# Optimization experiments

Hardware: AMD Instinct MI355X
Metric: run time of the kernel (lower is better)

## Reference

```python
import jax, jax.numpy as jnp
import numpy as np

RES = 32  # voxel grid resolution per axis (cfg.MODEL.NEURAL_POINTS.VOXEL_RES)


def upsample_ac(x, s):
    """Bilinear upsample with align_corners=True. x: [B,C,h,w] -> [B,C,h*s,w*s]."""
    if s == 1:
        return x
    B, C, h, w = x.shape
    H, W = h * s, w * s
    ys = jnp.arange(H, dtype=x.dtype) * ((h - 1) / (H - 1))
    xs = jnp.arange(W, dtype=x.dtype) * ((w - 1) / (W - 1))
    y0 = jnp.floor(ys).astype(jnp.int32)
    x0 = jnp.floor(xs).astype(jnp.int32)
    y1 = jnp.minimum(y0 + 1, h - 1)
    x1 = jnp.minimum(x0 + 1, w - 1)
    wy = (ys - y0.astype(x.dtype))[:, None]  # [H,1]
    wx = (xs - x0.astype(x.dtype))[None, :]  # [1,W]
    top = x[:, :, y0, :]
    bot = x[:, :, y1, :]
    a = top[..., x0]; b = top[..., x1]; c = bot[..., x0]; d = bot[..., x1]
    return (a * (1 - wx) + b * wx) * (1 - wy) + (c * (1 - wx) + d * wx) * wy


def vox_closest(pos):
    """construct_vox_points_closest: per occupied voxel, index of point closest to
    the voxel's point centroid. pos: [N,3] -> [RES^3] int32 indices."""
    N = pos.shape[0]
    Vn = RES ** 3
    mn = pos.min(0)
    mx = pos.max(0)
    vsz = (mx - mn) / RES  # obtain_voxel_size_based_grid_res
    coord = jnp.clip(jnp.floor((pos - mn) / vsz).astype(jnp.int32), 0, RES - 1)
    vid = (coord[:, 0] * RES + coord[:, 1]) * RES + coord[:, 2]  # [N]
    cnt = jax.ops.segment_sum(jnp.ones((N,), pos.dtype), vid, Vn)
    cen = jax.ops.segment_sum(pos, vid, Vn) / jnp.maximum(cnt, 1.0)[:, None]
    d = jnp.sum((pos - cen[vid]) ** 2, axis=-1)  # [N] dist^2 to own-voxel centroid
    dmin = jax.ops.segment_min(d, vid, Vn)
    cand = jnp.where(d <= dmin[vid], jnp.arange(N, dtype=jnp.int32), N)
    midx = jax.ops.segment_min(cand, vid, Vn)
    return jnp.where(midx >= N, 0, midx)  # guard (rare) empty voxels


def reference(rgb, f1, f2, f3, points_pos, points_dir, W1, b1, W2, b2, points_mask):
    V, _, H, W = rgb.shape
    N = V * H * W
    C = 59
    # valid_index = where(points_mask == 1) (mask is all ones -> identity gather)
    valid = jnp.nonzero(points_mask[0] == 1, size=N, fill_value=0)[0]
    pos = points_pos[0, valid]          # [N,3]
    pdir = points_dir[0, valid]         # [N,3]
    # project_point_feats: upsample each pyramid level to full res, concat channels
    ups = [upsample_ac(rgb, 1), upsample_ac(f1, 2), upsample_ac(f2, 4), upsample_ac(f3, 8)]
    pif = jnp.concatenate(ups, axis=1)                       # [V,59,H,W]
    pif = jnp.transpose(pif, (0, 2, 3, 1)).reshape(N, C)     # [N,59]
    color = jax.lax.stop_gradient(jnp.transpose(rgb, (0, 2, 3, 1)).reshape(N, 3))
    pif = pif[valid]
    color = color[valid]
    emb = jnp.concatenate([pif, pdir], axis=-1)              # [N,62]
    midx = vox_closest(pos)                                  # [32768]
    sel_emb = emb[midx]
    sel_pos = pos[midx]
    sel_color = color[midx]
    sel_dir = pdir[midx]
    # point_mlp (premlp_init): 62 -> 256 -> 256
    h = jax.nn.relu(sel_emb @ W1 + b1)
    points_embedding = h @ W2 + b2
    return points_embedding, sel_pos, sel_color, sel_dir


def setup_inputs() -> dict:
    key = jax.random.key(0)
    ks = jax.random.split(key, 10)
    V, H, W = 8, 240, 320
    N = V * H * W
    return {
        "rgb": jax.random.uniform(ks[0], (V, 3, H, W), jnp.float32),
        "f1": jax.random.normal(ks[1], (V, 8, H // 2, W // 2), jnp.float32),
        "f2": jax.random.normal(ks[2], (V, 16, H // 4, W // 4), jnp.float32),
        "f3": jax.random.normal(ks[3], (V, 32, H // 8, W // 8), jnp.float32),
        "points_pos": jax.random.uniform(ks[4], (1, N, 3), jnp.float32),
        "points_dir": jax.random.normal(ks[5], (1, N, 3), jnp.float32),
        "W1": jax.random.normal(ks[6], (62, 256), jnp.float32) * 0.05,
        "b1": jnp.zeros((256,), jnp.float32),
        "W2": jax.random.normal(ks[7], (256, 256), jnp.float32) * 0.05,
        "b2": jnp.zeros((256,), jnp.float32),
        "points_mask": jnp.ones((1, N), jnp.int32),
    }
```

## Files before the change

kernel.cpp:

```cpp
#include <hip/hip_runtime.h>
#include <hip/hip_bf16.h>
#include <limits.h>
#include <stddef.h>

#define NPTS   614400
#define RESV   32
#define NVOX   (RESV*RESV*RESV)
#define IMG_H  240
#define IMG_W  320
#define IMG_HW (IMG_H*IMG_W)
#define INF    __builtin_inff()
#define CAP    64
#define SPILLCAP 4096

typedef __attribute__((ext_vector_type(8))) short short8;
typedef __attribute__((ext_vector_type(4))) short s16x4;
typedef __attribute__((ext_vector_type(4))) float f32x4;
typedef float f32x4u __attribute__((ext_vector_type(4), aligned(4)));

__device__ __forceinline__ float fadd_(float a, float b){
#pragma clang fp contract(off)
  return a + b;
}
__device__ __forceinline__ float fsub_(float a, float b){
#pragma clang fp contract(off)
  return a - b;
}
__device__ __forceinline__ float fmul_(float a, float b){
#pragma clang fp contract(off)
  return a * b;
}
__device__ __forceinline__ float fdiv_(float a, float b){
#pragma clang fp contract(off)
  return a / b;
}

__device__ __forceinline__ short f2bf(float x){
  __hip_bfloat16 h = __float2bfloat16(x);
  return *reinterpret_cast<short*>(&h);
}

__global__ void k_prep(int* __restrict__ cnt, int* __restrict__ spillcnt,
                       const float* __restrict__ W1, const float* __restrict__ W2,
                       short* __restrict__ W1t, short* __restrict__ W2t,
                       const float* __restrict__ pos,
                       f32x4* __restrict__ pmin, f32x4* __restrict__ pmax){
  int gid = blockIdx.x*blockDim.x + threadIdx.x;
  if (gid < NVOX) cnt[gid] = 0;
  if (gid == 0) *spillcnt = 0;
  if (gid < 256*64){
    int n = gid >> 6, k = gid & 63;
    W1t[gid] = (k < 62) ? f2bf(W1[k*256 + n]) : (short)0;
  } else if (gid < 256*64 + 256*256){
    int j = gid - 256*64;
    int n = j >> 8, k = j & 255;
    W2t[j] = f2bf(W2[k*256 + n]);
  }

  const f32x4* p4 = (const f32x4*)pos;
  float mn[3] = {  INF,  INF,  INF };
  float mx[3] = { -INF, -INF, -INF };
  int stride = gridDim.x*blockDim.x;
  for (int t = gid; t < NPTS/4; t += stride){
    f32x4 a = p4[3*t+0], b = p4[3*t+1], c = p4[3*t+2];
    mn[0] = fminf(mn[0], fminf(fminf(a.x, a.w), fminf(b.z, c.y)));
    mx[0] = fmaxf(mx[0], fmaxf(fmaxf(a.x, a.w), fmaxf(b.z, c.y)));
    mn[1] = fminf(mn[1], fminf(fminf(a.y, b.x), fminf(b.w, c.z)));
    mx[1] = fmaxf(mx[1], fmaxf(fmaxf(a.y, b.x), fmaxf(b.w, c.z)));
    mn[2] = fminf(mn[2], fminf(fminf(a.z, b.y), fminf(c.x, c.w)));
    mx[2] = fmaxf(mx[2], fmaxf(fmaxf(a.z, b.y), fmaxf(c.x, c.w)));
  }
  #pragma unroll
  for (int off = 32; off >= 1; off >>= 1){
    #pragma unroll
    for (int c = 0; c < 3; c++){
      mn[c] = fminf(mn[c], __shfl_down(mn[c], off, 64));
      mx[c] = fmaxf(mx[c], __shfl_down(mx[c], off, 64));
    }
  }
  __shared__ float smn[4][3], smx[4][3];
  int lane = threadIdx.x & 63, w = threadIdx.x >> 6;
  if (lane == 0){
    #pragma unroll
    for (int c = 0; c < 3; c++){ smn[w][c] = mn[c]; smx[w][c] = mx[c]; }
  }
  __syncthreads();
  if (threadIdx.x == 0){
    f32x4 a, b;
    a.x = fminf(fminf(smn[0][0], smn[1][0]), fminf(smn[2][0], smn[3][0]));
    a.y = fminf(fminf(smn[0][1], smn[1][1]), fminf(smn[2][1], smn[3][1]));
    a.z = fminf(fminf(smn[0][2], smn[1][2]), fminf(smn[2][2], smn[3][2]));
    a.w = 0.f;
    b.x = fmaxf(fmaxf(smx[0][0], smx[1][0]), fmaxf(smx[2][0], smx[3][0]));
    b.y = fmaxf(fmaxf(smx[0][1], smx[1][1]), fmaxf(smx[2][1], smx[3][1]));
    b.z = fmaxf(fmaxf(smx[0][2], smx[1][2]), fmaxf(smx[2][2], smx[3][2]));
    b.w = 0.f;
    pmin[blockIdx.x] = a;
    pmax[blockIdx.x] = b;
  }
}

__device__ __forceinline__ void reduce_minmax(const f32x4* __restrict__ pmin,
                                              const f32x4* __restrict__ pmax,
                                              float mn[3], float vsz[3]){
  int t = threadIdx.x;
  f32x4 a = pmin[t], b = pmin[t+256];
  f32x4 c = pmax[t], d = pmax[t+256];
  float lmn[3] = { fminf(a.x,b.x), fminf(a.y,b.y), fminf(a.z,b.z) };
  float lmx[3] = { fmaxf(c.x,d.x), fmaxf(c.y,d.y), fmaxf(c.z,d.z) };
  #pragma unroll
  for (int off = 32; off >= 1; off >>= 1){
    #pragma unroll
    for (int k = 0; k < 3; k++){
      lmn[k] = fminf(lmn[k], __shfl_xor(lmn[k], off, 64));
      lmx[k] = fmaxf(lmx[k], __shfl_xor(lmx[k], off, 64));
    }
  }
  __shared__ float smn[4][3], smx[4][3];
  int lane = t & 63, w = t >> 6;
  if (lane == 0){
    #pragma unroll
    for (int k = 0; k < 3; k++){ smn[w][k] = lmn[k]; smx[w][k] = lmx[k]; }
  }
  __syncthreads();
  #pragma unroll
  for (int k = 0; k < 3; k++){
    mn[k] = fminf(fminf(smn[0][k], smn[1][k]), fminf(smn[2][k], smn[3][k]));
    float mx = fmaxf(fmaxf(smx[0][k], smx[1][k]), fmaxf(smx[2][k], smx[3][k]));
    vsz[k] = fdiv_(fsub_(mx, mn[k]), 32.0f);
  }
}

__global__ void k_scatter(const float* __restrict__ pos,
                          const f32x4* __restrict__ pmin, const f32x4* __restrict__ pmax,
                          int* __restrict__ cnt, int* __restrict__ slots,
                          int* __restrict__ spillcnt, int2* __restrict__ spill){
  float mn[3], vsz[3];
  reduce_minmax(pmin, pmax, mn, vsz);

  int t = blockIdx.x*blockDim.x + threadIdx.x;
  const f32x4* p4 = (const f32x4*)pos;
  f32x4 a = p4[3*t+0], b = p4[3*t+1], c = p4[3*t+2];
  float X[4] = {a.x, a.w, b.z, c.y};
  float Y[4] = {a.y, b.x, b.w, c.z};
  float Z[4] = {a.z, b.y, c.x, c.w};
  #pragma unroll
  for (int j = 0; j < 4; j++){
    int i = 4*t + j;
    float P[3] = {X[j], Y[j], Z[j]};
    int v = 0;
    #pragma unroll
    for (int k = 0; k < 3; k++){
      float tt = fdiv_(fsub_(P[k], mn[k]), vsz[k]);
      int cc = (int)floorf(tt);
      cc = min(max(cc, 0), RESV-1);
      v = v*RESV + cc;
    }
    int p = atomicAdd(&cnt[v], 1);
    if (p < CAP){
      slots[v*CAP + p] = i;
    } else {
      int sp = atomicAdd(spillcnt, 1);
      if (sp < SPILLCAP){ int2 e; e.x = v; e.y = i; spill[sp] = e; }
    }
  }
}

__launch_bounds__(256)
__global__ void k_voxfull(const int* __restrict__ cnt, const int* __restrict__ slots,
                          const int* __restrict__ spillcnt, const int2* __restrict__ spill,
                          const float* __restrict__ pos,
                          const float* __restrict__ pdir, const float* __restrict__ rgb,
                          const float* __restrict__ f1, const float* __restrict__ f2,
                          const float* __restrict__ f3,
                          float* __restrict__ selpos, float* __restrict__ selcol,
                          float* __restrict__ seldir, short* __restrict__ emb){
  int lane = threadIdx.x & 63;
  int v = blockIdx.x*4 + (threadIdx.x >> 6);
  int n = cnt[v];
  int m = 0;
  unsigned long long ball = 0;
  float px = 0.f, py = 0.f, pz = 0.f;

  if (n > CAP){
    if (lane == 0){
      int sc = min(*spillcnt, SPILLCAP);
      float sx = 0.f, sy = 0.f, sz = 0.f; int last = -1;
      for (int i = 0; i < n; i++){
        int best = INT_MAX;
        for (int j = 0; j < CAP; j++){
          int id = slots[v*CAP + j];
          if (id > last && id < best) best = id;
        }
        for (int j = 0; j < sc; j++){
          int2 e = spill[j];
          if (e.x == v && e.y > last && e.y < best) best = e.y;
        }
        sx = fadd_(sx, pos[3*best+0]);
        sy = fadd_(sy, pos[3*best+1]);
        sz = fadd_(sz, pos[3*best+2]);
        last = best;
      }
      float cf = (float)n;
      float cx = fdiv_(sx, cf), cy = fdiv_(sy, cf), cz = fdiv_(sz, cf);
      float dmin = INF; int mm = 0;
      for (int j = 0; j < CAP + sc; j++){
        int id; int ok = 1;
        if (j < CAP) id = slots[v*CAP + j];
        else { int2 e = spill[j-CAP]; ok = (e.x == v); id = e.y; }
        if (!ok) continue;
        float dx = fsub_(pos[3*id+0], cx);
        float dy = fsub_(pos[3*id+1], cy);
        float dz = fsub_(pos[3*id+2], cz);
        float d  = fadd_(fadd_(fmul_(dx,dx), fmul_(dy,dy)), fmul_(dz,dz));
        if (d < dmin || (d == dmin && id < mm)){ dmin = d; mm = id; }
      }
      m = mm;
    }
    m = __shfl(m, 0, 64);
  } else {
    int key = INT_MAX;
    float gx = 0.f, gy = 0.f, gz = 0.f;
    if (lane < n){
      key = slots[v*CAP + lane];
      if (key < NPTS-1){
        f32x4u q = *(const f32x4u*)&pos[3*key];
        gx = q.x; gy = q.y; gz = q.z;
      } else {
        gx = pos[3*key+0]; gy = pos[3*key+1]; gz = pos[3*key+2];
      }
    }
    int src = lane;
    #pragma unroll
    for (int k = 2; k <= 64; k <<= 1){
      #pragma unroll
      for (int j = k >> 1; j >= 1; j >>= 1){
        int ok = __shfl_xor(key, j, 64);
        int os = __shfl_xor(src, j, 64);
        bool up    = ((lane & k) == 0);
        bool lower = ((lane & j) == 0);
        bool sw = (lower == up) ? (ok < key) : (ok > key);
        if (sw){ key = ok; src = os; }
      }
    }
    px = __shfl(gx, src, 64);
    py = __shfl(gy, src, 64);
    pz = __shfl(gz, src, 64);

    float sx = 0.f, sy = 0.f, sz = 0.f;
    for (int i = 0; i < n; i++){
      sx = fadd_(sx, __shfl(px, i, 64));
      sy = fadd_(sy, __shfl(py, i, 64));
      sz = fadd_(sz, __shfl(pz, i, 64));
    }
    float cf = fmaxf((float)n, 1.0f);
    float cx = fdiv_(sx, cf), cy = fdiv_(sy, cf), cz = fdiv_(sz, cf);

    float bd = INF; int bi = 0;
    if (lane < n){
      float dx = fsub_(px, cx), dy = fsub_(py, cy), dz = fsub_(pz, cz);
      bd = fadd_(fadd_(fmul_(dx,dx), fmul_(dy,dy)), fmul_(dz,dz));
      bi = key;
    }
    #pragma unroll
    for (int off = 32; off >= 1; off >>= 1){
      float od = __shfl_xor(bd, off, 64);
      int   oi = __shfl_xor(bi, off, 64);
      if (od < bd || (od == bd && oi < bi)){ bd = od; bi = oi; }
    }
    m = bi;
    ball = __ballot(lane < n && key == m);
  }

  float wx_ = 0.f, wy_ = 0.f, wz_ = 0.f;
  if (ball){
    int wl = (int)(__ffsll((long long)ball) - 1);
    wx_ = __shfl(px, wl, 64);
    wy_ = __shfl(py, wl, 64);
    wz_ = __shfl(pz, wl, 64);
  }

  int img = m / IMG_HW;
  int rem = m - img*IMG_HW;
  int y = rem / IMG_W;
  int x = rem - y*IMG_W;
  int ch = lane;
  float val;
  if (ch < 3){
    val = rgb[((img*3 + ch)*IMG_H + y)*IMG_W + x];
    selcol[3*v+ch] = val;
    float sp = ball ? ((ch == 0) ? wx_ : (ch == 1) ? wy_ : wz_) : pos[3*m+ch];
    selpos[3*v+ch] = sp;
  } else if (ch < 59){
    int lvl = (ch >= 27) ? 2 : ((ch >= 11) ? 1 : 0);
    const float* f = (lvl == 0) ? f1 : ((lvl == 1) ? f2 : f3);
    int c   = ch - ((lvl == 0) ? 3 : ((lvl == 1) ? 11 : 27));
    int C   = 8 << lvl;
    int h   = 120 >> lvl, w = 160 >> lvl;
    float ry = (lvl == 0) ? (119.0f/239.0f) : ((lvl == 1) ? (59.0f/239.0f) : (29.0f/239.0f));
    float rx = (lvl == 0) ? (159.0f/319.0f) : ((lvl == 1) ? (79.0f/319.0f) : (39.0f/319.0f));
    float ys = (float)y * ry;
    float xs = (float)x * rx;
    int y0 = (int)floorf(ys);
    int x0 = (int)floorf(xs);
    int y1 = min(y0+1, h-1);
    int x1 = min(x0+1, w-1);
    float wy = ys - (float)y0;
    float wx = xs - (float)x0;
    const float* plane = f + ((size_t)img*C + c)*(size_t)(h*w);
    float aa = plane[y0*w + x0];
    float bb = plane[y0*w + x1];
    float cc = plane[y1*w + x0];
    float dd = plane[y1*w + x1];
    val = (aa*(1.f-wx) + bb*wx)*(1.f-wy) + (cc*(1.f-wx) + dd*wx)*wy;
  } else if (ch < 62){
    val = pdir[3*m + (ch-59)];
    seldir[3*v+(ch-59)] = val;
  } else {
    val = 0.f;
  }
  emb[(size_t)v*64 + ch] = f2bf(val);
}

#define MLP_BLOCKS 512
#define MLP_TILES  (NVOX/16/MLP_BLOCKS)
__launch_bounds__(256, 2)
__global__ void k_mlp(const short* __restrict__ emb, const short* __restrict__ W1t,
                      const float* __restrict__ b1f, const short* __restrict__ W2t,
                      const float* __restrict__ b2f, float* __restrict__ out){
  __shared__ short Hs[16][264];
  int t    = threadIdx.x;
  int lane = t & 63;
  int wv   = t >> 6;
  int m    = lane & 15;
  int q    = lane >> 4;

  short8 w1f[4][2], w2f[4][8];
  float  b1r[4][4], b2r[4];
  #pragma unroll
  for (int nt = 0; nt < 4; nt++){
    int n = wv*64 + nt*16 + m;
    #pragma unroll
    for (int kq = 0; kq < 2; kq++)
      w1f[nt][kq] = *(const short8*)&W1t[(size_t)n*64 + kq*32 + q*8];
    #pragma unroll
    for (int kq = 0; kq < 8; kq++)
      w2f[nt][kq] = *(const short8*)&W2t[(size_t)n*256 + kq*32 + q*8];
    #pragma unroll
    for (int i = 0; i < 4; i++)
      b1r[nt][i] = b1f[wv*64 + nt*16 + q*4 + i];
    b2r[nt] = b2f[n];
  }

  for (int tt = 0; tt < MLP_TILES; tt++){
    int row0 = (blockIdx.x*MLP_TILES + tt)*16;

    short8 ef0 = *(const short8*)&emb[(size_t)(row0 + m)*64 + q*8];
    short8 ef1 = *(const short8*)&emb[(size_t)(row0 + m)*64 + 32 + q*8];

    #pragma unroll
    for (int nt = 0; nt < 4; nt++){
      f32x4 c = {0.f, 0.f, 0.f, 0.f};
      c = __builtin_amdgcn_mfma_f32_16x16x32_bf16(w1f[nt][0], ef0, c, 0, 0, 0);
      c = __builtin_amdgcn_mfma_f32_16x16x32_bf16(w1f[nt][1], ef1, c, 0, 0, 0);
      s16x4 hv;
      #pragma unroll
      for (int i = 0; i < 4; i++)
        hv[i] = f2bf(fmaxf(c[i] + b1r[nt][i], 0.f));
      *(s16x4*)&Hs[m][wv*64 + nt*16 + q*4] = hv;
    }
    __syncthreads();

    f32x4 acc[4] = {{0,0,0,0},{0,0,0,0},{0,0,0,0},{0,0,0,0}};
    #pragma unroll
    for (int kq = 0; kq < 8; kq++){
      short8 af = *(const short8*)&Hs[m][kq*32 + q*8];
      #pragma unroll
      for (int nt = 0; nt < 4; nt++)
        acc[nt] = __builtin_amdgcn_mfma_f32_16x16x32_bf16(af, w2f[nt][kq], acc[nt], 0, 0, 0);
    }
    __syncthreads();

    #pragma unroll
    for (int nt = 0; nt < 4; nt++){
      int n = wv*64 + nt*16 + m;
      #pragma unroll
      for (int i = 0; i < 4; i++)
        out[(size_t)(row0 + q*4 + i)*256 + n] = acc[nt][i] + b2r[nt];
    }
  }
}

extern "C" void kernel_launch(void* const* d_in, const int* in_sizes, int n_in,
                              void* d_out, int out_size, void* d_ws, size_t ws_size,
                              hipStream_t stream){
  const float* rgb  = (const float*)d_in[0];
  const float* f1   = (const float*)d_in[1];
  const float* f2   = (const float*)d_in[2];
  const float* f3   = (const float*)d_in[3];
  const float* pos  = (const float*)d_in[4];
  const float* pdir = (const float*)d_in[5];
  const float* W1   = (const float*)d_in[6];
  const float* b1   = (const float*)d_in[7];
  const float* W2   = (const float*)d_in[8];
  const float* b2   = (const float*)d_in[9];

  float* out      = (float*)d_out;
  float* out_emb  = out;
  float* out_pos  = out + (size_t)NVOX*256;
  float* out_col  = out_pos + (size_t)NVOX*3;
  float* out_dir  = out_col + (size_t)NVOX*3;

  char* w = (char*)d_ws;
  int*   spillcnt = (int*)w;       w += 64;
  f32x4* pmin     = (f32x4*)w;     w += (size_t)512*16;
  f32x4* pmax     = (f32x4*)w;     w += (size_t)512*16;
  int*   cnt      = (int*)w;       w += (size_t)NVOX*4;
  short* W1t      = (short*)w;     w += (size_t)256*64*2;
  short* W2t      = (short*)w;     w += (size_t)256*256*2;
  short* emb      = (short*)w;     w += (size_t)NVOX*64*2;
  int2*  spill    = (int2*)w;      w += (size_t)SPILLCAP*8;
  int*   slots    = (int*)w;       w += (size_t)NVOX*CAP*4;

  k_prep    <<<512,    256, 0, stream>>>(cnt, spillcnt, W1, W2, W1t, W2t, pos, pmin, pmax);
  k_scatter <<<NPTS/1024, 256, 0, stream>>>(pos, pmin, pmax, cnt, slots, spillcnt, spill);
  k_voxfull <<<NVOX/4, 256, 0, stream>>>(cnt, slots, spillcnt, spill,
                                         pos, pdir, rgb, f1, f2, f3,
                                         out_pos, out_col, out_dir, emb);
  k_mlp     <<<MLP_BLOCKS, 256, 0, stream>>>(emb, W1t, b1, W2t, b2, out_emb);
}
```

Baseline: 198.2 us.

## Split voxel kernel and bucket voxels by selected point index for gather locality

```diff
diff --git a/kernel.cpp b/kernel.cpp
--- a/kernel.cpp
+++ b/kernel.cpp
@@ -12,6 +12,9 @@
 #define INF    __builtin_inff()
 #define CAP    64
 #define SPILLCAP 4096
+#define NB     150
+#define CAPB   448
+#define OCAP   2048
 
 typedef __attribute__((ext_vector_type(8))) short short8;
 typedef __attribute__((ext_vector_type(4))) short s16x4;
@@ -40,14 +43,16 @@
   return *reinterpret_cast<short*>(&h);
 }
 
-__global__ void k_prep(int* __restrict__ cnt, int* __restrict__ spillcnt,
+__global__ void k_prep(int* __restrict__ cnt, int* __restrict__ ctrs,
+                       int* __restrict__ bcnt,
                        const float* __restrict__ W1, const float* __restrict__ W2,
                        short* __restrict__ W1t, short* __restrict__ W2t,
                        const float* __restrict__ pos,
                        f32x4* __restrict__ pmin, f32x4* __restrict__ pmax){
   int gid = blockIdx.x*blockDim.x + threadIdx.x;
   if (gid < NVOX) cnt[gid] = 0;
-  if (gid == 0) *spillcnt = 0;
+  if (gid < NB) bcnt[gid] = 0;
+  if (gid < 2) ctrs[gid] = 0;
   if (gid < 256*64){
     int n = gid >> 6, k = gid & 63;
     W1t[gid] = (k < 62) ? f2bf(W1[k*256 + n]) : (short)0;
@@ -134,7 +139,7 @@
 __global__ void k_scatter(const float* __restrict__ pos,
                           const f32x4* __restrict__ pmin, const f32x4* __restrict__ pmax,
                           int* __restrict__ cnt, int* __restrict__ slots,
-                          int* __restrict__ spillcnt, int2* __restrict__ spill){
+                          int* __restrict__ ctrs, int2* __restrict__ spill){
   float mn[3], vsz[3];
   reduce_minmax(pmin, pmax, mn, vsz);
 
@@ -160,21 +165,19 @@
     if (p < CAP){
       slots[v*CAP + p] = i;
     } else {
-      int sp = atomicAdd(spillcnt, 1);
+      int sp = atomicAdd(&ctrs[0], 1);
       if (sp < SPILLCAP){ int2 e; e.x = v; e.y = i; spill[sp] = e; }
     }
   }
 }
 
 __launch_bounds__(256)
-__global__ void k_voxfull(const int* __restrict__ cnt, const int* __restrict__ slots,
-                          const int* __restrict__ spillcnt, const int2* __restrict__ spill,
-                          const float* __restrict__ pos,
-                          const float* __restrict__ pdir, const float* __restrict__ rgb,
-                          const float* __restrict__ f1, const float* __restrict__ f2,
-                          const float* __restrict__ f3,
-                          float* __restrict__ selpos, float* __restrict__ selcol,
-                          float* __restrict__ seldir, short* __restrict__ emb){
+__global__ void k_voxA(const int* __restrict__ cnt, const int* __restrict__ slots,
+                       const int* __restrict__ ctrs, const int2* __restrict__ spill,
+                       const float* __restrict__ pos,
+                       float* __restrict__ selpos, int* __restrict__ midx,
+                       int* __restrict__ bcnt, int* __restrict__ blist,
+                       int* __restrict__ octr, int* __restrict__ olist){
   int lane = threadIdx.x & 63;
   int v = blockIdx.x*4 + (threadIdx.x >> 6);
   int n = cnt[v];
@@ -184,7 +187,7 @@
 
   if (n > CAP){
     if (lane == 0){
-      int sc = min(*spillcnt, SPILLCAP);
+      int sc = min(ctrs[0], SPILLCAP);
       float sx = 0.f, sy = 0.f, sz = 0.f; int last = -1;
       for (int i = 0; i < n; i++){
         int best = INT_MAX;
@@ -279,6 +282,46 @@
     wy_ = __shfl(py, wl, 64);
     wz_ = __shfl(pz, wl, 64);
   }
+  if (lane < 3){
+    float sp = ball ? ((lane == 0) ? wx_ : (lane == 1) ? wy_ : wz_) : pos[3*m+lane];
+    selpos[3*v+lane] = sp;
+  }
+  if (lane == 0){
+    midx[v] = m;
+    int b = m >> 12;
+    int s = atomicAdd(&bcnt[b], 1);
+    if (s < CAPB) blist[b*CAPB + s] = v;
+    else {
+      int o = atomicAdd(octr, 1);
+      if (o < OCAP) olist[o] = v;
+    }
+  }
+}
+
+__launch_bounds__(256)
+__global__ void k_voxB(const int* __restrict__ bcnt, const int* __restrict__ blist,
+                       const int* __restrict__ octr, const int* __restrict__ olist,
+                       const int* __restrict__ midx,
+                       const float* __restrict__ pdir, const float* __restrict__ rgb,
+                       const float* __restrict__ f1, const float* __restrict__ f2,
+                       const float* __restrict__ f3,
+                       float* __restrict__ selcol, float* __restrict__ seldir,
+                       short* __restrict__ emb){
+  int wv = threadIdx.x >> 6;
+  int lane = threadIdx.x & 63;
+  int v;
+  if (blockIdx.x < NB*CAPB/4){
+    int g = blockIdx.x*4 + wv;
+    int b = g / CAPB;
+    int s = g - b*CAPB;
+    if (s >= min(bcnt[b], CAPB)) return;
+    v = blist[b*CAPB + s];
+  } else {
+    int o = (blockIdx.x - NB*CAPB/4)*4 + wv;
+    if (o >= min(*octr, OCAP)) return;
+    v = olist[o];
+  }
+  int m = midx[v];
 
   int img = m / IMG_HW;
   int rem = m - img*IMG_HW;
@@ -289,8 +332,6 @@
   if (ch < 3){
     val = rgb[((img*3 + ch)*IMG_H + y)*IMG_W + x];
     selcol[3*v+ch] = val;
-    float sp = ball ? ((ch == 0) ? wx_ : (ch == 1) ? wy_ : wz_) : pos[3*m+ch];
-    selpos[3*v+ch] = sp;
   } else if (ch < 59){
     int lvl = (ch >= 27) ? 2 : ((ch >= 11) ? 1 : 0);
     const float* f = (lvl == 0) ? f1 : ((lvl == 1) ? f2 : f3);
@@ -412,20 +453,26 @@
   float* out_dir  = out_col + (size_t)NVOX*3;
 
   char* w = (char*)d_ws;
-  int*   spillcnt = (int*)w;       w += 64;
+  int*   ctrs     = (int*)w;       w += 64;
   f32x4* pmin     = (f32x4*)w;     w += (size_t)512*16;
   f32x4* pmax     = (f32x4*)w;     w += (size_t)512*16;
   int*   cnt      = (int*)w;       w += (size_t)NVOX*4;
+  int*   midx     = (int*)w;       w += (size_t)NVOX*4;
   short* W1t      = (short*)w;     w += (size_t)256*64*2;
   short* W2t      = (short*)w;     w += (size_t)256*256*2;
   short* emb      = (short*)w;     w += (size_t)NVOX*64*2;
   int2*  spill    = (int2*)w;      w += (size_t)SPILLCAP*8;
+  int*   bcnt     = (int*)w;       w += (size_t)((NB*4 + 63)/64)*64;
+  int*   blist    = (int*)w;       w += (size_t)NB*CAPB*4;
+  int*   olist    = (int*)w;       w += (size_t)OCAP*4;
   int*   slots    = (int*)w;       w += (size_t)NVOX*CAP*4;
 
-  k_prep    <<<512,    256, 0, stream>>>(cnt, spillcnt, W1, W2, W1t, W2t, pos, pmin, pmax);
-  k_scatter <<<NPTS/1024, 256, 0, stream>>>(pos, pmin, pmax, cnt, slots, spillcnt, spill);
-  k_voxfull <<<NVOX/4, 256, 0, stream>>>(cnt, slots, spillcnt, spill,
-                                         pos, pdir, rgb, f1, f2, f3,
-                                         out_pos, out_col, out_dir, emb);
+  k_prep    <<<512,    256, 0, stream>>>(cnt, ctrs, bcnt, W1, W2, W1t, W2t, pos, pmin, pmax);
+  k_scatter <<<NPTS/1024, 256, 0, stream>>>(pos, pmin, pmax, cnt, slots, ctrs, spill);
+  k_voxA    <<<NVOX/4, 256, 0, stream>>>(cnt, slots, ctrs, spill, pos,
+                                         out_pos, midx, bcnt, blist, &ctrs[1], olist);
+  k_voxB    <<<NB*CAPB/4 + OCAP/4, 256, 0, stream>>>(bcnt, blist, &ctrs[1], olist, midx,
+                                         pdir, rgb, f1, f2, f3,
+                                         out_col, out_dir, emb);
   k_mlp     <<<MLP_BLOCKS, 256, 0, stream>>>(emb, W1t, b1, W2t, b2, out_emb);
 }
```

New measurement: 257.7 us. 1.3x slower.
